# Performance work log

Measured on AMD Instinct MI355X. Metric: run time of the kernel, lower is better.

## Reference

```python
import jax, jax.numpy as jnp
import numpy as np


def _pointnet(x, w1, b1, w2, b2, w3, b3):
    # x: [B, P, 5] -> pointwise MLP then max-pool over points -> [B, 64]
    h = jax.nn.relu(x @ w1.T + b1)
    h = jax.nn.relu(h @ w2.T + b2)
    h = h @ w3.T + b3
    return h.max(axis=1)


def _lstm_layer(x, wih, whh, bih, bhh):
    # x: [B, T, D]; PyTorch gate order i, f, g, o
    B = x.shape[0]
    H = whh.shape[1]
    def step(carry, xt):
        h, c = carry
        g = xt @ wih.T + bih + h @ whh.T + bhh
        i, f, gg, o = jnp.split(g, 4, axis=-1)
        c = jax.nn.sigmoid(f) * c + jax.nn.sigmoid(i) * jnp.tanh(gg)
        h = jax.nn.sigmoid(o) * jnp.tanh(c)
        return (h, c), h
    init = (jnp.zeros((B, H), x.dtype), jnp.zeros((B, H), x.dtype))
    (h_last, _), hs = jax.lax.scan(step, init, jnp.swapaxes(x, 0, 1))
    return jnp.swapaxes(hs, 0, 1), h_last


def _edge_conv(h, mask, wt, bt, wp, bp):
    # DGL EdgeConv: h_i' = max_{j in N(i)} theta(h_j - h_i) + phi(h_i)
    # theta is linear -> max_j (Th_j) - Th_i + b_theta + phi(h_i)
    Th = h @ wt.T                       # [V,128]
    Ph = h @ wp.T + bp                  # [V,128]
    neigh_max = jnp.max(jnp.where(mask[:, :, None], Th[None, :, :], -jnp.inf), axis=1)
    return neigh_max - Th + bt + Ph


def _edge_regr(e, w1, b1, w2, b2):
    return jax.nn.sigmoid(jax.nn.relu(e @ w1.T + b1) @ w2.T + b2)


def _affinity(h, N, M, er_w1, er_b1, er_w2, er_b2):
    # faithful to source: edges[i*M+j] = h[j] - h[i]  (j indexes first M rows, as in the code)
    E = (h[None, :M, :] - h[:N, None, :]).reshape(N * M, -1)
    return _edge_regr(E, er_w1, er_b1, er_w2, er_b2).reshape(N, M)


def setup_inputs() -> dict:
    key = jax.random.key(0)
    ks = iter(jax.random.split(key, 40))
    N, M, P, T = 256, 256, 512, 10
    lin = lambda k, o, i: (jax.random.normal(k, (o, i), jnp.float32) / np.sqrt(i)).astype(jnp.float32)
    inp = {
        'det_pts': jax.random.normal(next(ks), (N, P, 5), jnp.float32),
        'det_boxes': jax.random.normal(next(ks), (N, 9), jnp.float32),
        'track_pts': jax.random.normal(next(ks), (M, P, 5), jnp.float32),
        'track_boxes': jax.random.normal(next(ks), (M, T, 9), jnp.float32),
        'adj': jax.random.randint(next(ks), (N + M, N + M), 0, 2, jnp.int32),
        'pn_w1': lin(next(ks), 64, 5), 'pn_b1': jnp.zeros((64,), jnp.float32),
        'pn_w2': lin(next(ks), 128, 64), 'pn_b2': jnp.zeros((128,), jnp.float32),
        'pn_w3': lin(next(ks), 64, 128), 'pn_b3': jnp.zeros((64,), jnp.float32),
        'dm_w1': lin(next(ks), 32, 9), 'dm_b1': jnp.zeros((32,), jnp.float32),
        'dm_w2': lin(next(ks), 64, 32), 'dm_b2': jnp.zeros((64,), jnp.float32),
        'l0_wih': lin(next(ks), 256, 9), 'l0_whh': lin(next(ks), 256, 64),
        'l0_bih': jnp.zeros((256,), jnp.float32), 'l0_bhh': jnp.zeros((256,), jnp.float32),
        'l1_wih': lin(next(ks), 256, 64), 'l1_whh': lin(next(ks), 256, 64),
        'l1_bih': jnp.zeros((256,), jnp.float32), 'l1_bhh': jnp.zeros((256,), jnp.float32),
        'gc_wt': jnp.stack([lin(next(ks), 128, 128) for _ in range(4)]),
        'gc_bt': jnp.zeros((4, 128), jnp.float32),
        'gc_wp': jnp.stack([lin(next(ks), 128, 128) for _ in range(4)]),
        'gc_bp': jnp.zeros((4, 128), jnp.float32),
        'er_w1': lin(next(ks), 64, 128), 'er_b1': jnp.zeros((64,), jnp.float32),
        'er_w2': lin(next(ks), 1, 64), 'er_b2': jnp.zeros((1,), jnp.float32),
    }
    return inp


def reference(det_pts, det_boxes, track_pts, track_boxes, adj,
              pn_w1, pn_b1, pn_w2, pn_b2, pn_w3, pn_b3,
              dm_w1, dm_b1, dm_w2, dm_b2,
              l0_wih, l0_whh, l0_bih, l0_bhh,
              l1_wih, l1_whh, l1_bih, l1_bhh,
              gc_wt, gc_bt, gc_wp, gc_bp,
              er_w1, er_b1, er_w2, er_b2):
    N, M = det_pts.shape[0], track_pts.shape[0]
    V = N + M
    # appearance features (shared PointNet)
    det_app = _pointnet(det_pts, pn_w1, pn_b1, pn_w2, pn_b2, pn_w3, pn_b3)    # [N,64]
    trk_app = _pointnet(track_pts, pn_w1, pn_b1, pn_w2, pn_b2, pn_w3, pn_b3)  # [M,64]
    # motion features
    det_mot = jax.nn.relu(det_boxes @ dm_w1.T + dm_b1) @ dm_w2.T + dm_b2      # [N,64]
    hs0, _ = _lstm_layer(track_boxes, l0_wih, l0_whh, l0_bih, l0_bhh)
    _, trk_mot = _lstm_layer(hs0, l1_wih, l1_whh, l1_bih, l1_bhh)             # [M,64]
    h = jnp.concatenate([
        jnp.concatenate([det_app, det_mot], axis=1),
        jnp.concatenate([trk_app, trk_mot], axis=1)], axis=0)                 # [V,128]
    # neighbor-source mask: edge i->j for adj[i,j]!=0, plus self-loops
    mask = (adj.T != 0) | jnp.eye(V, dtype=bool)                              # mask[i,j]: j is source neighbor of i
    aff1 = None
    for k in range(4):
        h = jax.nn.relu(_edge_conv(h, mask, gc_wt[k], gc_bt[k], gc_wp[k], gc_bp[k]))
        if k == 0:
            aff1 = _affinity(h, N, M, er_w1, er_b1, er_w2, er_b2)
    aff_final = _affinity(h, N, M, er_w1, er_b1, er_w2, er_b2)
    return jnp.stack([aff1, aff_final])  # [2, N, M]
```

## Files before the change

### kernel.cpp

```cpp
#include <hip/hip_runtime.h>
#include <math.h>

#define NDET 256
#define NTRK 256
#define NV   512
#define PPTS 512

typedef short bf16x8 __attribute__((ext_vector_type(8)));
typedef float f32x4  __attribute__((ext_vector_type(4)));

__device__ __forceinline__ float sigf(float x) { return 1.f / (1.f + __expf(-x)); }
__device__ __forceinline__ float ftanh(float x) {
    const float xc = fmaxf(fminf(x, 15.f), -15.f);
    const float e = __expf(2.f * xc);
    return (e - 1.f) / (e + 1.f);
}

__device__ __forceinline__ short f2bf(float f) {
    unsigned u = __float_as_uint(f);
    u += 0x7fffu + ((u >> 16) & 1u);
    return (short)(u >> 16);
}
__device__ __forceinline__ unsigned pack2bf(float lo, float hi) {
    return (unsigned)(unsigned short)f2bf(lo) | ((unsigned)(unsigned short)f2bf(hi) << 16);
}
__device__ __forceinline__ bf16x8 load_frag_bf16(const float* __restrict__ src) {
    const float4 a = *(const float4*)src;
    const float4 b = *(const float4*)(src + 4);
    bf16x8 r;
    r[0] = f2bf(a.x); r[1] = f2bf(a.y); r[2] = f2bf(a.z); r[3] = f2bf(a.w);
    r[4] = f2bf(b.x); r[5] = f2bf(b.y); r[6] = f2bf(b.z); r[7] = f2bf(b.w);
    return r;
}

__global__ __launch_bounds__(256) void pointnet_kernel(
    const float* __restrict__ det_pts, const float* __restrict__ track_pts,
    const float* __restrict__ w1, const float* __restrict__ b1,
    const float* __restrict__ w2, const float* __restrict__ b2,
    const float* __restrict__ w3, const float* __restrict__ b3,
    const float* __restrict__ det_boxes,
    const float* __restrict__ dw1, const float* __restrict__ db1,
    const float* __restrict__ dw2, const float* __restrict__ db2,
    float* __restrict__ hout)
{
    __shared__ __align__(16) short sH1[64][72];
    __shared__ __align__(16) short sH2[64][136];
    __shared__ __align__(16) float sX[320];
    __shared__ float sW1f[64][6];
    __shared__ float sB1[64];
    __shared__ float sbox[9];
    __shared__ float sh32[32];

    const int t  = threadIdx.x;
    const int b  = blockIdx.x;
    const int w  = t >> 6;
    const int ln = t & 15;
    const int kq = (t >> 4) & 3;
    const float* x = (b < NDET) ? (det_pts + (size_t)b * PPTS * 5)
                                : (track_pts + (size_t)(b - NDET) * PPTS * 5);

    for (int i = t; i < 320; i += 256) sW1f[i / 5][i % 5] = w1[i];
    if (t < 64) sB1[t] = b1[t];

    bf16x8 bf2[2][2];
#pragma unroll
    for (int nt = 0; nt < 2; ++nt)
#pragma unroll
        for (int Kt = 0; Kt < 2; ++Kt)
            bf2[nt][Kt] = load_frag_bf16(w2 + (size_t)(32 * w + 16 * nt + ln) * 64 + kq * 8 + 32 * Kt);
    bf16x8 bf3[4];
#pragma unroll
    for (int Kt = 0; Kt < 4; ++Kt)
        bf3[Kt] = load_frag_bf16(w3 + (size_t)(16 * w + ln) * 128 + kq * 8 + 32 * Kt);
    float bn[2];
#pragma unroll
    for (int nt = 0; nt < 2; ++nt) bn[nt] = b2[32 * w + 16 * nt + ln];
    __syncthreads();

    float runmax[4] = {-1e30f, -1e30f, -1e30f, -1e30f};

    const int pt = t & 63;
    for (int c = 0; c < PPTS / 64; ++c) {
        for (int i = t; i < 320; i += 256) sX[i] = x[c * 320 + i];
        __syncthreads();
        {
            float xv[5];
#pragma unroll
            for (int k = 0; k < 5; ++k) xv[k] = sX[pt * 5 + k];
#pragma unroll
            for (int jj = 0; jj < 8; ++jj) {
                const int d0 = w * 16 + 2 * jj;
                float a0 = sB1[d0], a1 = sB1[d0 + 1];
#pragma unroll
                for (int k = 0; k < 5; ++k) {
                    a0 = fmaf(xv[k], sW1f[d0][k], a0);
                    a1 = fmaf(xv[k], sW1f[d0 + 1][k], a1);
                }
                *(unsigned*)&sH1[pt][d0] = pack2bf(fmaxf(a0, 0.f), fmaxf(a1, 0.f));
            }
        }
        __syncthreads();
        {
            bf16x8 af[4][2];
#pragma unroll
            for (int Mt = 0; Mt < 4; ++Mt)
#pragma unroll
                for (int Kt = 0; Kt < 2; ++Kt)
                    af[Mt][Kt] = *(const bf16x8*)&sH1[16 * Mt + ln][kq * 8 + 32 * Kt];
#pragma unroll
            for (int Mt = 0; Mt < 4; ++Mt) {
#pragma unroll
                for (int nt = 0; nt < 2; ++nt) {
                    f32x4 cacc = {0.f, 0.f, 0.f, 0.f};
                    cacc = __builtin_amdgcn_mfma_f32_16x16x32_bf16(af[Mt][0], bf2[nt][0], cacc, 0, 0, 0);
                    cacc = __builtin_amdgcn_mfma_f32_16x16x32_bf16(af[Mt][1], bf2[nt][1], cacc, 0, 0, 0);
                    const int col = 32 * w + 16 * nt + ln;
#pragma unroll
                    for (int r = 0; r < 4; ++r)
                        sH2[16 * Mt + kq * 4 + r][col] = f2bf(fmaxf(cacc[r] + bn[nt], 0.f));
                }
            }
        }
        __syncthreads();
        {
#pragma unroll
            for (int Mt = 0; Mt < 4; ++Mt) {
                f32x4 cacc = {0.f, 0.f, 0.f, 0.f};
#pragma unroll
                for (int Kt = 0; Kt < 4; ++Kt) {
                    const bf16x8 a = *(const bf16x8*)&sH2[16 * Mt + ln][kq * 8 + 32 * Kt];
                    cacc = __builtin_amdgcn_mfma_f32_16x16x32_bf16(a, bf3[Kt], cacc, 0, 0, 0);
                }
#pragma unroll
                for (int r = 0; r < 4; ++r) runmax[r] = fmaxf(runmax[r], cacc[r]);
            }
        }
        __syncthreads();
    }

    float rm = fmaxf(fmaxf(runmax[0], runmax[1]), fmaxf(runmax[2], runmax[3]));
    rm = fmaxf(rm, __shfl_xor(rm, 16));
    rm = fmaxf(rm, __shfl_xor(rm, 32));
    if ((t & 63) < 16) {
        const int n = 16 * w + ln;
        hout[b * 128 + n] = rm + b3[n];
    }

    if (b < NDET) {
        if (t < 9) sbox[t] = det_boxes[b * 9 + t];
        __syncthreads();
        if (t < 32) {
            float a = db1[t];
#pragma unroll
            for (int k = 0; k < 9; ++k) a = fmaf(dw1[t * 9 + k], sbox[k], a);
            sh32[t] = fmaxf(a, 0.f);
        }
        __syncthreads();
        if (t < 64) {
            float a = db2[t];
#pragma unroll
            for (int k = 0; k < 32; ++k) a = fmaf(dw2[t * 32 + k], sh32[k], a);
            hout[b * 128 + 64 + t] = a;
        }
    }
}

__global__ __launch_bounds__(256, 1) void lstm_kernel(
    const float* __restrict__ track_boxes,
    const float* __restrict__ wih0, const float* __restrict__ whh0,
    const float* __restrict__ bih0, const float* __restrict__ bhh0,
    const float* __restrict__ wih1, const float* __restrict__ whh1,
    const float* __restrict__ bih1, const float* __restrict__ bhh1,
    float* __restrict__ hout)
{
    __shared__ float sx[90];
    __shared__ float sg[256];
    __shared__ __align__(16) float sh0[64];
    __shared__ __align__(16) float sh1[64];

    const int t = threadIdx.x;
    const int m = blockIdx.x;
    const int u = t & 63;

    if (t < 90) sx[t] = track_boxes[m * 90 + t];
    if (t < 64) { sh0[t] = 0.f; sh1[t] = 0.f; }

    float w0[9];
#pragma unroll
    for (int k = 0; k < 9; ++k) w0[k] = wih0[t * 9 + k];
    float4 wr0[16], wi1[16], wr1[16];
    {
        const float4* p0 = (const float4*)(whh0 + t * 64);
        const float4* p1 = (const float4*)(wih1 + t * 64);
        const float4* p2 = (const float4*)(whh1 + t * 64);
#pragma unroll
        for (int k = 0; k < 16; ++k) { wr0[k] = p0[k]; wi1[k] = p1[k]; wr1[k] = p2[k]; }
    }
    const float bias0 = bih0[t] + bhh0[t];
    const float bias1 = bih1[t] + bhh1[t];

    float c0 = 0.f, c1 = 0.f, h1reg = 0.f;
    __syncthreads();

    for (int s = 0; s < 10; ++s) {
        {
            float acc0 = bias0, acc1 = 0.f, acc2 = 0.f, acc3 = 0.f;
#pragma unroll
            for (int k = 0; k < 9; ++k) acc0 = fmaf(w0[k], sx[s * 9 + k], acc0);
            const float4* hv = (const float4*)sh0;
#pragma unroll
            for (int k = 0; k < 16; k += 4) {
                float4 hA = hv[k], hB = hv[k + 1], hC = hv[k + 2], hD = hv[k + 3];
                acc0 = fmaf(wr0[k].x, hA.x, acc0); acc0 = fmaf(wr0[k].y, hA.y, acc0);
                acc0 = fmaf(wr0[k].z, hA.z, acc0); acc0 = fmaf(wr0[k].w, hA.w, acc0);
                acc1 = fmaf(wr0[k+1].x, hB.x, acc1); acc1 = fmaf(wr0[k+1].y, hB.y, acc1);
                acc1 = fmaf(wr0[k+1].z, hB.z, acc1); acc1 = fmaf(wr0[k+1].w, hB.w, acc1);
                acc2 = fmaf(wr0[k+2].x, hC.x, acc2); acc2 = fmaf(wr0[k+2].y, hC.y, acc2);
                acc2 = fmaf(wr0[k+2].z, hC.z, acc2); acc2 = fmaf(wr0[k+2].w, hC.w, acc2);
                acc3 = fmaf(wr0[k+3].x, hD.x, acc3); acc3 = fmaf(wr0[k+3].y, hD.y, acc3);
                acc3 = fmaf(wr0[k+3].z, hD.z, acc3); acc3 = fmaf(wr0[k+3].w, hD.w, acc3);
            }
            sg[t] = (acc0 + acc1) + (acc2 + acc3);
        }
        __syncthreads();
        if (t < 64) {
            const float gi = sg[u], gf = sg[64 + u], gg = sg[128 + u], go = sg[192 + u];
            c0 = sigf(gf) * c0 + sigf(gi) * ftanh(gg);
            sh0[u] = sigf(go) * ftanh(c0);
        }
        __syncthreads();
        {
            float acc0 = bias1, acc1 = 0.f, acc2 = 0.f, acc3 = 0.f;
            const float4* xv = (const float4*)sh0;
            const float4* hv = (const float4*)sh1;
#pragma unroll
            for (int k = 0; k < 16; k += 4) {
                float4 xA = xv[k], xB = xv[k + 1], xC = xv[k + 2], xD = xv[k + 3];
                acc0 = fmaf(wi1[k].x, xA.x, acc0); acc0 = fmaf(wi1[k].y, xA.y, acc0);
                acc0 = fmaf(wi1[k].z, xA.z, acc0); acc0 = fmaf(wi1[k].w, xA.w, acc0);
                acc1 = fmaf(wi1[k+1].x, xB.x, acc1); acc1 = fmaf(wi1[k+1].y, xB.y, acc1);
                acc1 = fmaf(wi1[k+1].z, xB.z, acc1); acc1 = fmaf(wi1[k+1].w, xB.w, acc1);
                acc2 = fmaf(wi1[k+2].x, xC.x, acc2); acc2 = fmaf(wi1[k+2].y, xC.y, acc2);
                acc2 = fmaf(wi1[k+2].z, xC.z, acc2); acc2 = fmaf(wi1[k+2].w, xC.w, acc2);
                acc3 = fmaf(wi1[k+3].x, xD.x, acc3); acc3 = fmaf(wi1[k+3].y, xD.y, acc3);
                acc3 = fmaf(wi1[k+3].z, xD.z, acc3); acc3 = fmaf(wi1[k+3].w, xD.w, acc3);
            }
#pragma unroll
            for (int k = 0; k < 16; k += 4) {
                float4 hA = hv[k], hB = hv[k + 1], hC = hv[k + 2], hD = hv[k + 3];
                acc0 = fmaf(wr1[k].x, hA.x, acc0); acc0 = fmaf(wr1[k].y, hA.y, acc0);
                acc0 = fmaf(wr1[k].z, hA.z, acc0); acc0 = fmaf(wr1[k].w, hA.w, acc0);
                acc1 = fmaf(wr1[k+1].x, hB.x, acc1); acc1 = fmaf(wr1[k+1].y, hB.y, acc1);
                acc1 = fmaf(wr1[k+1].z, hB.z, acc1); acc1 = fmaf(wr1[k+1].w, hB.w, acc1);
                acc2 = fmaf(wr1[k+2].x, hC.x, acc2); acc2 = fmaf(wr1[k+2].y, hC.y, acc2);
                acc2 = fmaf(wr1[k+2].z, hC.z, acc2); acc2 = fmaf(wr1[k+2].w, hC.w, acc2);
                acc3 = fmaf(wr1[k+3].x, hD.x, acc3); acc3 = fmaf(wr1[k+3].y, hD.y, acc3);
                acc3 = fmaf(wr1[k+3].z, hD.z, acc3); acc3 = fmaf(wr1[k+3].w, hD.w, acc3);
            }
            sg[t] = (acc0 + acc1) + (acc2 + acc3);
        }
        __syncthreads();
        if (t < 64) {
            const float gi = sg[u], gf = sg[64 + u], gg = sg[128 + u], go = sg[192 + u];
            c1 = sigf(gf) * c1 + sigf(gi) * ftanh(gg);
            h1reg = sigf(go) * ftanh(c1);
            sh1[u] = h1reg;
        }
        __syncthreads();
    }

    if (t < 64) hout[(size_t)(NDET + m) * 128 + 64 + u] = h1reg;
}

__global__ __launch_bounds__(128) void econv_gemm_kernel(
    const float* __restrict__ hin, const float* __restrict__ wt,
    const float* __restrict__ wp, const float* __restrict__ bp,
    float* __restrict__ Th, float* __restrict__ Ph)
{
    __shared__ __align__(16) float srow[128];
    const int t = threadIdx.x, v = blockIdx.x;
    srow[t] = hin[v * 128 + t];
    __syncthreads();
    const float4* hr = (const float4*)srow;
    const float4* wtr = (const float4*)(wt + t * 128);
    const float4* wpr = (const float4*)(wp + t * 128);
    float aT = 0.f, aP = bp[t];
#pragma unroll 8
    for (int k = 0; k < 32; ++k) {
        const float4 h = hr[k];
        const float4 a = wtr[k];
        aT = fmaf(a.x, h.x, aT); aT = fmaf(a.y, h.y, aT);
        aT = fmaf(a.z, h.z, aT); aT = fmaf(a.w, h.w, aT);
        const float4 b = wpr[k];
        aP = fmaf(b.x, h.x, aP); aP = fmaf(b.y, h.y, aP);
        aP = fmaf(b.z, h.z, aP); aP = fmaf(b.w, h.w, aP);
    }
    Th[v * 128 + t] = aT;
    Ph[v * 128 + t] = aP;
}

__global__ __launch_bounds__(128) void econv_fused_kernel(
    const int* __restrict__ adj, const float* __restrict__ Th,
    const float* __restrict__ Ph, const float* __restrict__ bt,
    const float* __restrict__ wtn, const float* __restrict__ wpn,
    const float* __restrict__ bpn,
    const float* __restrict__ erw1, float* __restrict__ uu,
    float* __restrict__ Thn, float* __restrict__ Phn)
{
    __shared__ float sneg[NV];
    __shared__ __align__(16) float4 sred[4][32];
    __shared__ __align__(16) float sh[128];

    const int t = threadIdx.x, i = blockIdx.x;
    const int l32 = t & 31, grp = t >> 5;

    for (int j = t; j < NV; j += 128)
        sneg[j] = ((adj[j * NV + i] != 0) || (j == i)) ? 0.f : -3e38f;

    const float thi = Th[i * 128 + t];
    const float phi = Ph[i * 128 + t];
    const float btv = bt[t];
    __syncthreads();

    float4 mx = {-3e38f, -3e38f, -3e38f, -3e38f};
    const float* __restrict__ thp = Th + 4 * l32;
#pragma unroll 4
    for (int jb = 0; jb < NV; jb += 16) {
        float4 v[4];
#pragma unroll
        for (int jj = 0; jj < 4; ++jj)
            v[jj] = *(const float4*)&thp[(size_t)(jb + 4 * jj + grp) * 128];
#pragma unroll
        for (int jj = 0; jj < 4; ++jj) {
            const float s = sneg[jb + 4 * jj + grp];
            mx.x = fmaxf(mx.x, v[jj].x + s);
            mx.y = fmaxf(mx.y, v[jj].y + s);
            mx.z = fmaxf(mx.z, v[jj].z + s);
            mx.w = fmaxf(mx.w, v[jj].w + s);
        }
    }
    sred[grp][l32] = mx;
    __syncthreads();

    const float* rf = (const float*)sred;
    const float m = fmaxf(fmaxf(rf[t], rf[128 + t]), fmaxf(rf[256 + t], rf[384 + t]));
    sh[t] = fmaxf(m - thi + btv + phi, 0.f);
    __syncthreads();

    const float4* hr = (const float4*)sh;
    if (wtn) {
        const float4* wtr = (const float4*)(wtn + t * 128);
        const float4* wpr = (const float4*)(wpn + t * 128);
        float aT = 0.f, aP = bpn[t];
#pragma unroll 8
        for (int k = 0; k < 32; ++k) {
            const float4 h = hr[k];
            const float4 a = wtr[k];
            aT = fmaf(a.x, h.x, aT); aT = fmaf(a.y, h.y, aT);
            aT = fmaf(a.z, h.z, aT); aT = fmaf(a.w, h.w, aT);
            const float4 b = wpr[k];
            aP = fmaf(b.x, h.x, aP); aP = fmaf(b.y, h.y, aP);
            aP = fmaf(b.z, h.z, aP); aP = fmaf(b.w, h.w, aP);
        }
        Thn[i * 128 + t] = aT;
        Phn[i * 128 + t] = aP;
    }
    if (erw1 && i < NDET && t < 64) {
        const float4* wr = (const float4*)(erw1 + t * 128);
        float a = 0.f;
#pragma unroll 8
        for (int k = 0; k < 32; ++k) {
            const float4 h = hr[k], wv = wr[k];
            a = fmaf(wv.x, h.x, a); a = fmaf(wv.y, h.y, a);
            a = fmaf(wv.z, h.z, a); a = fmaf(wv.w, h.w, a);
        }
        uu[i * 64 + t] = a;
    }
}

__global__ __launch_bounds__(256) void edge_kernel(
    const float* __restrict__ uu1, const float* __restrict__ uu2,
    const float* __restrict__ b1, const float* __restrict__ w2,
    const float* __restrict__ b2, float* __restrict__ out)
{
    __shared__ float sui[64], sw2[64], sb1[64];
    const int t = threadIdx.x, blk = blockIdx.x;
    const float* u = (blk < NDET) ? uu1 : uu2;
    float* o = (blk < NDET) ? out : out + NDET * NTRK;
    const int i = blk & (NDET - 1);
    if (t < 64) { sui[t] = u[i * 64 + t]; sw2[t] = w2[t]; sb1[t] = b1[t]; }
    __syncthreads();
    const float4* ur = (const float4*)(u + t * 64);
    float a = b2[0];
#pragma unroll
    for (int k = 0; k < 16; ++k) {
        const float4 uv = ur[k];
        const int k4 = k * 4;
        a = fmaf(sw2[k4 + 0], fmaxf(uv.x - sui[k4 + 0] + sb1[k4 + 0], 0.f), a);
        a = fmaf(sw2[k4 + 1], fmaxf(uv.y - sui[k4 + 1] + sb1[k4 + 1], 0.f), a);
        a = fmaf(sw2[k4 + 2], fmaxf(uv.z - sui[k4 + 2] + sb1[k4 + 2], 0.f), a);
        a = fmaf(sw2[k4 + 3], fmaxf(uv.w - sui[k4 + 3] + sb1[k4 + 3], 0.f), a);
    }
    o[i * 256 + t] = 1.f / (1.f + __expf(-a));
}

extern "C" void kernel_launch(void* const* d_in, const int* in_sizes, int n_in,
                              void* d_out, int out_size, void* d_ws, size_t ws_size,
                              hipStream_t stream)
{
    const float* det_pts     = (const float*)d_in[0];
    const float* det_boxes   = (const float*)d_in[1];
    const float* track_pts   = (const float*)d_in[2];
    const float* track_boxes = (const float*)d_in[3];
    const int*   adj         = (const int*)d_in[4];
    const float* pn_w1 = (const float*)d_in[5],  *pn_b1 = (const float*)d_in[6];
    const float* pn_w2 = (const float*)d_in[7],  *pn_b2 = (const float*)d_in[8];
    const float* pn_w3 = (const float*)d_in[9],  *pn_b3 = (const float*)d_in[10];
    const float* dm_w1 = (const float*)d_in[11], *dm_b1 = (const float*)d_in[12];
    const float* dm_w2 = (const float*)d_in[13], *dm_b2 = (const float*)d_in[14];
    const float* l0_wih = (const float*)d_in[15], *l0_whh = (const float*)d_in[16];
    const float* l0_bih = (const float*)d_in[17], *l0_bhh = (const float*)d_in[18];
    const float* l1_wih = (const float*)d_in[19], *l1_whh = (const float*)d_in[20];
    const float* l1_bih = (const float*)d_in[21], *l1_bhh = (const float*)d_in[22];
    const float* gc_wt = (const float*)d_in[23], *gc_bt = (const float*)d_in[24];
    const float* gc_wp = (const float*)d_in[25], *gc_bp = (const float*)d_in[26];
    const float* er_w1 = (const float*)d_in[27], *er_b1 = (const float*)d_in[28];
    const float* er_w2 = (const float*)d_in[29], *er_b2 = (const float*)d_in[30];
    float* out = (float*)d_out;

    float* hA  = (float*)d_ws;
    float* Th  = hA  + NV * 128;
    float* Ph  = Th  + NV * 128;
    float* Th2 = Ph  + NV * 128;
    float* Ph2 = Th2 + NV * 128;
    float* uu1 = Ph2 + NV * 128;
    float* uu2 = uu1 + NDET * 64;

    pointnet_kernel<<<NV, 256, 0, stream>>>(det_pts, track_pts,
        pn_w1, pn_b1, pn_w2, pn_b2, pn_w3, pn_b3,
        det_boxes, dm_w1, dm_b1, dm_w2, dm_b2, hA);
    lstm_kernel<<<NTRK, 256, 0, stream>>>(track_boxes,
        l0_wih, l0_whh, l0_bih, l0_bhh, l1_wih, l1_whh, l1_bih, l1_bhh, hA);

    econv_gemm_kernel<<<NV, 128, 0, stream>>>(hA, gc_wt, gc_wp, gc_bp, Th, Ph);

    const size_t WSZ = 128 * 128;
    econv_fused_kernel<<<NV, 128, 0, stream>>>(adj, Th, Ph, gc_bt,
        gc_wt + WSZ, gc_wp + WSZ, gc_bp + 128, er_w1, uu1, Th2, Ph2);
    econv_fused_kernel<<<NV, 128, 0, stream>>>(adj, Th2, Ph2, gc_bt + 128,
        gc_wt + 2 * WSZ, gc_wp + 2 * WSZ, gc_bp + 256, nullptr, nullptr, Th, Ph);
    econv_fused_kernel<<<NV, 128, 0, stream>>>(adj, Th, Ph, gc_bt + 256,
        gc_wt + 3 * WSZ, gc_wp + 3 * WSZ, gc_bp + 384, nullptr, nullptr, Th2, Ph2);
    econv_fused_kernel<<<NV, 128, 0, stream>>>(adj, Th2, Ph2, gc_bt + 384,
        nullptr, nullptr, nullptr, er_w1, uu2, nullptr, nullptr);

    edge_kernel<<<NV, 256, 0, stream>>>(uu1, uu2, er_b1, er_w2, er_b2, out);
}
```

Baseline: 244.1 us.

## Merge edge-conv and affinity stages into one cooperative kernel with grid syncs

Replaces the six launches for the graph-conv layers and the affinity edge kernel with a single cooperative kernel of 512 blocks. Grid-wide syncs separate the layers, and each block keeps its adjacency mask in shared memory across all four layers, so it is read once instead of four times. Each block's own Th/Ph row stays in registers. The aim is to remove launch overhead and repeated mask loads. In exchange it adds five grid barriers and a cooperative launch, and the final edge stage now runs with 128 threads doing two outputs each.

```diff
diff --git a/kernel.cpp b/kernel.cpp
--- a/kernel.cpp
+++ b/kernel.cpp
@@ -1,5 +1,8 @@
 #include <hip/hip_runtime.h>
+#include <hip/hip_cooperative_groups.h>
 #include <math.h>
+
+namespace cg = cooperative_groups;
 
 #define NDET 256
 #define NTRK 256
@@ -272,86 +275,40 @@
     if (t < 64) hout[(size_t)(NDET + m) * 128 + 64 + u] = h1reg;
 }
 
-__global__ __launch_bounds__(128) void econv_gemm_kernel(
-    const float* __restrict__ hin, const float* __restrict__ wt,
-    const float* __restrict__ wp, const float* __restrict__ bp,
-    float* __restrict__ Th, float* __restrict__ Ph)
+__global__ void backend_kernel(
+    const float* __restrict__ hA, const int* __restrict__ adj,
+    const float* __restrict__ gc_wt, const float* __restrict__ gc_bt,
+    const float* __restrict__ gc_wp, const float* __restrict__ gc_bp,
+    const float* __restrict__ er_w1, const float* __restrict__ er_b1,
+    const float* __restrict__ er_w2, const float* __restrict__ er_b2,
+    float* __restrict__ ThA, float* __restrict__ PhA,
+    float* __restrict__ ThB, float* __restrict__ PhB,
+    float* __restrict__ uu1, float* __restrict__ uu2,
+    float* __restrict__ out)
 {
+    cg::grid_group grid = cg::this_grid();
+
     __shared__ __align__(16) float srow[128];
-    const int t = threadIdx.x, v = blockIdx.x;
-    srow[t] = hin[v * 128 + t];
-    __syncthreads();
-    const float4* hr = (const float4*)srow;
-    const float4* wtr = (const float4*)(wt + t * 128);
-    const float4* wpr = (const float4*)(wp + t * 128);
-    float aT = 0.f, aP = bp[t];
-#pragma unroll 8
-    for (int k = 0; k < 32; ++k) {
-        const float4 h = hr[k];
-        const float4 a = wtr[k];
-        aT = fmaf(a.x, h.x, aT); aT = fmaf(a.y, h.y, aT);
-        aT = fmaf(a.z, h.z, aT); aT = fmaf(a.w, h.w, aT);
-        const float4 b = wpr[k];
-        aP = fmaf(b.x, h.x, aP); aP = fmaf(b.y, h.y, aP);
-        aP = fmaf(b.z, h.z, aP); aP = fmaf(b.w, h.w, aP);
-    }
-    Th[v * 128 + t] = aT;
-    Ph[v * 128 + t] = aP;
-}
-
-__global__ __launch_bounds__(128) void econv_fused_kernel(
-    const int* __restrict__ adj, const float* __restrict__ Th,
-    const float* __restrict__ Ph, const float* __restrict__ bt,
-    const float* __restrict__ wtn, const float* __restrict__ wpn,
-    const float* __restrict__ bpn,
-    const float* __restrict__ erw1, float* __restrict__ uu,
-    float* __restrict__ Thn, float* __restrict__ Phn)
-{
     __shared__ float sneg[NV];
     __shared__ __align__(16) float4 sred[4][32];
     __shared__ __align__(16) float sh[128];
+    __shared__ float sui[64], sw2v[64], sb1v[64];
 
     const int t = threadIdx.x, i = blockIdx.x;
     const int l32 = t & 31, grp = t >> 5;
+    const size_t WSZ = 128 * 128;
 
     for (int j = t; j < NV; j += 128)
         sneg[j] = ((adj[j * NV + i] != 0) || (j == i)) ? 0.f : -3e38f;
 
-    const float thi = Th[i * 128 + t];
-    const float phi = Ph[i * 128 + t];
-    const float btv = bt[t];
+    srow[t] = hA[(size_t)i * 128 + t];
     __syncthreads();
-
-    float4 mx = {-3e38f, -3e38f, -3e38f, -3e38f};
-    const float* __restrict__ thp = Th + 4 * l32;
-#pragma unroll 4
-    for (int jb = 0; jb < NV; jb += 16) {
-        float4 v[4];
-#pragma unroll
-        for (int jj = 0; jj < 4; ++jj)
-            v[jj] = *(const float4*)&thp[(size_t)(jb + 4 * jj + grp) * 128];
-#pragma unroll
-        for (int jj = 0; jj < 4; ++jj) {
-            const float s = sneg[jb + 4 * jj + grp];
-            mx.x = fmaxf(mx.x, v[jj].x + s);
-            mx.y = fmaxf(mx.y, v[jj].y + s);
-            mx.z = fmaxf(mx.z, v[jj].z + s);
-            mx.w = fmaxf(mx.w, v[jj].w + s);
-        }
-    }
-    sred[grp][l32] = mx;
-    __syncthreads();
-
-    const float* rf = (const float*)sred;
-    const float m = fmaxf(fmaxf(rf[t], rf[128 + t]), fmaxf(rf[256 + t], rf[384 + t]));
-    sh[t] = fmaxf(m - thi + btv + phi, 0.f);
-    __syncthreads();
-
-    const float4* hr = (const float4*)sh;
-    if (wtn) {
-        const float4* wtr = (const float4*)(wtn + t * 128);
-        const float4* wpr = (const float4*)(wpn + t * 128);
-        float aT = 0.f, aP = bpn[t];
+    float thi, phi;
+    {
+        const float4* hr = (const float4*)srow;
+        const float4* wtr = (const float4*)(gc_wt + (size_t)t * 128);
+        const float4* wpr = (const float4*)(gc_wp + (size_t)t * 128);
+        float aT = 0.f, aP = gc_bp[t];
 #pragma unroll 8
         for (int k = 0; k < 32; ++k) {
             const float4 h = hr[k];
@@ -362,46 +319,103 @@
             aP = fmaf(b.x, h.x, aP); aP = fmaf(b.y, h.y, aP);
             aP = fmaf(b.z, h.z, aP); aP = fmaf(b.w, h.w, aP);
         }
-        Thn[i * 128 + t] = aT;
-        Phn[i * 128 + t] = aP;
-    }
-    if (erw1 && i < NDET && t < 64) {
-        const float4* wr = (const float4*)(erw1 + t * 128);
-        float a = 0.f;
+        ThA[(size_t)i * 128 + t] = aT;
+        PhA[(size_t)i * 128 + t] = aP;
+        thi = aT; phi = aP;
+    }
+    grid.sync();
+
+    float* Tin = ThA; float* Tout = ThB;
+    float* Pout = PhB;
+    for (int k = 0; k < 4; ++k) {
+        const bool active = (k < 3) || (i < NDET);
+        if (active) {
+            const float btv = gc_bt[k * 128 + t];
+            float4 mx = {-3e38f, -3e38f, -3e38f, -3e38f};
+            const float* __restrict__ thp = Tin + 4 * l32;
+#pragma unroll 4
+            for (int jb = 0; jb < NV; jb += 16) {
+                float4 v[4];
+#pragma unroll
+                for (int jj = 0; jj < 4; ++jj)
+                    v[jj] = *(const float4*)&thp[(size_t)(jb + 4 * jj + grp) * 128];
+#pragma unroll
+                for (int jj = 0; jj < 4; ++jj) {
+                    const float s = sneg[jb + 4 * jj + grp];
+                    mx.x = fmaxf(mx.x, v[jj].x + s);
+                    mx.y = fmaxf(mx.y, v[jj].y + s);
+                    mx.z = fmaxf(mx.z, v[jj].z + s);
+                    mx.w = fmaxf(mx.w, v[jj].w + s);
+                }
+            }
+            sred[grp][l32] = mx;
+            __syncthreads();
+
+            const float* rf = (const float*)sred;
+            const float m = fmaxf(fmaxf(rf[t], rf[128 + t]), fmaxf(rf[256 + t], rf[384 + t]));
+            sh[t] = fmaxf(m - thi + btv + phi, 0.f);
+            __syncthreads();
+
+            const float4* hr = (const float4*)sh;
+            if (k < 3) {
+                const float* wtn = gc_wt + (size_t)(k + 1) * WSZ;
+                const float* wpn = gc_wp + (size_t)(k + 1) * WSZ;
+                const float4* wtr = (const float4*)(wtn + (size_t)t * 128);
+                const float4* wpr = (const float4*)(wpn + (size_t)t * 128);
+                float aT = 0.f, aP = gc_bp[(k + 1) * 128 + t];
 #pragma unroll 8
-        for (int k = 0; k < 32; ++k) {
-            const float4 h = hr[k], wv = wr[k];
-            a = fmaf(wv.x, h.x, a); a = fmaf(wv.y, h.y, a);
-            a = fmaf(wv.z, h.z, a); a = fmaf(wv.w, h.w, a);
-        }
-        uu[i * 64 + t] = a;
-    }
-}
-
-__global__ __launch_bounds__(256) void edge_kernel(
-    const float* __restrict__ uu1, const float* __restrict__ uu2,
-    const float* __restrict__ b1, const float* __restrict__ w2,
-    const float* __restrict__ b2, float* __restrict__ out)
-{
-    __shared__ float sui[64], sw2[64], sb1[64];
-    const int t = threadIdx.x, blk = blockIdx.x;
-    const float* u = (blk < NDET) ? uu1 : uu2;
-    float* o = (blk < NDET) ? out : out + NDET * NTRK;
-    const int i = blk & (NDET - 1);
-    if (t < 64) { sui[t] = u[i * 64 + t]; sw2[t] = w2[t]; sb1[t] = b1[t]; }
+                for (int kk = 0; kk < 32; ++kk) {
+                    const float4 h = hr[kk];
+                    const float4 a = wtr[kk];
+                    aT = fmaf(a.x, h.x, aT); aT = fmaf(a.y, h.y, aT);
+                    aT = fmaf(a.z, h.z, aT); aT = fmaf(a.w, h.w, aT);
+                    const float4 b = wpr[kk];
+                    aP = fmaf(b.x, h.x, aP); aP = fmaf(b.y, h.y, aP);
+                    aP = fmaf(b.z, h.z, aP); aP = fmaf(b.w, h.w, aP);
+                }
+                Tout[(size_t)i * 128 + t] = aT;
+                Pout[(size_t)i * 128 + t] = aP;
+                thi = aT; phi = aP;
+            }
+            if ((k == 0 || k == 3) && i < NDET && t < 64) {
+                float* uu = (k == 0) ? uu1 : uu2;
+                const float4* wr = (const float4*)(er_w1 + (size_t)t * 128);
+                float a = 0.f;
+#pragma unroll 8
+                for (int kk = 0; kk < 32; ++kk) {
+                    const float4 h = hr[kk], wv = wr[kk];
+                    a = fmaf(wv.x, h.x, a); a = fmaf(wv.y, h.y, a);
+                    a = fmaf(wv.z, h.z, a); a = fmaf(wv.w, h.w, a);
+                }
+                uu[(size_t)i * 64 + t] = a;
+            }
+        }
+        float* tmp = Tin; Tin = Tout; Tout = tmp;
+        Pout = (Pout == PhB) ? PhA : PhB;
+        grid.sync();
+    }
+
+    const int row = i & (NDET - 1);
+    const float* u = (i < NDET) ? uu1 : uu2;
+    float* o = (i < NDET) ? out : out + NDET * NTRK;
+    if (t < 64) { sui[t] = u[row * 64 + t]; sw2v[t] = er_w2[t]; sb1v[t] = er_b1[t]; }
     __syncthreads();
-    const float4* ur = (const float4*)(u + t * 64);
-    float a = b2[0];
-#pragma unroll
-    for (int k = 0; k < 16; ++k) {
-        const float4 uv = ur[k];
-        const int k4 = k * 4;
-        a = fmaf(sw2[k4 + 0], fmaxf(uv.x - sui[k4 + 0] + sb1[k4 + 0], 0.f), a);
-        a = fmaf(sw2[k4 + 1], fmaxf(uv.y - sui[k4 + 1] + sb1[k4 + 1], 0.f), a);
-        a = fmaf(sw2[k4 + 2], fmaxf(uv.z - sui[k4 + 2] + sb1[k4 + 2], 0.f), a);
-        a = fmaf(sw2[k4 + 3], fmaxf(uv.w - sui[k4 + 3] + sb1[k4 + 3], 0.f), a);
-    }
-    o[i * 256 + t] = 1.f / (1.f + __expf(-a));
+#pragma unroll
+    for (int jj = 0; jj < 2; ++jj) {
+        const int j = t + 128 * jj;
+        const float4* ur = (const float4*)(u + (size_t)j * 64);
+        float a = er_b2[0];
+#pragma unroll
+        for (int k = 0; k < 16; ++k) {
+            const float4 uv = ur[k];
+            const int k4 = k * 4;
+            a = fmaf(sw2v[k4 + 0], fmaxf(uv.x - sui[k4 + 0] + sb1v[k4 + 0], 0.f), a);
+            a = fmaf(sw2v[k4 + 1], fmaxf(uv.y - sui[k4 + 1] + sb1v[k4 + 1], 0.f), a);
+            a = fmaf(sw2v[k4 + 2], fmaxf(uv.z - sui[k4 + 2] + sb1v[k4 + 2], 0.f), a);
+            a = fmaf(sw2v[k4 + 3], fmaxf(uv.w - sui[k4 + 3] + sb1v[k4 + 3], 0.f), a);
+        }
+        o[row * 256 + j] = 1.f / (1.f + __expf(-a));
+    }
 }
 
 extern "C" void kernel_launch(void* const* d_in, const int* in_sizes, int n_in,
@@ -442,17 +456,13 @@
     lstm_kernel<<<NTRK, 256, 0, stream>>>(track_boxes,
         l0_wih, l0_whh, l0_bih, l0_bhh, l1_wih, l1_whh, l1_bih, l1_bhh, hA);
 
-    econv_gemm_kernel<<<NV, 128, 0, stream>>>(hA, gc_wt, gc_wp, gc_bp, Th, Ph);
-
-    const size_t WSZ = 128 * 128;
-    econv_fused_kernel<<<NV, 128, 0, stream>>>(adj, Th, Ph, gc_bt,
-        gc_wt + WSZ, gc_wp + WSZ, gc_bp + 128, er_w1, uu1, Th2, Ph2);
-    econv_fused_kernel<<<NV, 128, 0, stream>>>(adj, Th2, Ph2, gc_bt + 128,
-        gc_wt + 2 * WSZ, gc_wp + 2 * WSZ, gc_bp + 256, nullptr, nullptr, Th, Ph);
-    econv_fused_kernel<<<NV, 128, 0, stream>>>(adj, Th, Ph, gc_bt + 256,
-        gc_wt + 3 * WSZ, gc_wp + 3 * WSZ, gc_bp + 384, nullptr, nullptr, Th2, Ph2);
-    econv_fused_kernel<<<NV, 128, 0, stream>>>(adj, Th2, Ph2, gc_bt + 384,
-        nullptr, nullptr, nullptr, er_w1, uu2, nullptr, nullptr);
-
-    edge_kernel<<<NV, 256, 0, stream>>>(uu1, uu2, er_b1, er_w2, er_b2, out);
-}
+    void* args[] = {
+        (void*)&hA, (void*)&adj,
+        (void*)&gc_wt, (void*)&gc_bt, (void*)&gc_wp, (void*)&gc_bp,
+        (void*)&er_w1, (void*)&er_b1, (void*)&er_w2, (void*)&er_b2,
+        (void*)&Th, (void*)&Ph, (void*)&Th2, (void*)&Ph2,
+        (void*)&uu1, (void*)&uu2, (void*)&out
+    };
+    hipLaunchCooperativeKernel((const void*)backend_kernel,
+                               dim3(NV), dim3(128), args, 0, stream);
+}
```

Result: slower. 518.5 us (+112.4%).

## Split PointNet across two blocks per object and widen edge-conv blocks to 256 threads

Applied to the files above, without the earlier changes.

PointNet now launches two blocks per object, each handling half of the points and writing a partial max without the bias. The combine step (max of the two halves plus b3) moves into econv_gemm_kernel's row load. The edge-conv fused kernel goes to 256 threads: the neighbor max is spread over 8 groups, and the Th and Ph projections are split across the two thread halves. The aim is more parallelism in both phases, which were latency-bound at 512 blocks. The cost is an extra partial-result buffer and a wider 8-way reduction.

```diff
diff --git a/kernel.cpp b/kernel.cpp
--- a/kernel.cpp
+++ b/kernel.cpp
@@ -37,11 +37,11 @@
     const float* __restrict__ det_pts, const float* __restrict__ track_pts,
     const float* __restrict__ w1, const float* __restrict__ b1,
     const float* __restrict__ w2, const float* __restrict__ b2,
-    const float* __restrict__ w3, const float* __restrict__ b3,
+    const float* __restrict__ w3,
     const float* __restrict__ det_boxes,
     const float* __restrict__ dw1, const float* __restrict__ db1,
     const float* __restrict__ dw2, const float* __restrict__ db2,
-    float* __restrict__ hout)
+    float* __restrict__ pp, float* __restrict__ hout)
 {
     __shared__ __align__(16) short sH1[64][72];
     __shared__ __align__(16) short sH2[64][136];
@@ -52,12 +52,14 @@
     __shared__ float sh32[32];
 
     const int t  = threadIdx.x;
-    const int b  = blockIdx.x;
+    const int bb = blockIdx.x >> 1;
+    const int s  = blockIdx.x & 1;
     const int w  = t >> 6;
     const int ln = t & 15;
     const int kq = (t >> 4) & 3;
-    const float* x = (b < NDET) ? (det_pts + (size_t)b * PPTS * 5)
-                                : (track_pts + (size_t)(b - NDET) * PPTS * 5);
+    const float* x = ((bb < NDET) ? (det_pts + (size_t)bb * PPTS * 5)
+                                  : (track_pts + (size_t)(bb - NDET) * PPTS * 5))
+                     + (size_t)s * 1280;
 
     for (int i = t; i < 320; i += 256) sW1f[i / 5][i % 5] = w1[i];
     if (t < 64) sB1[t] = b1[t];
@@ -80,7 +82,7 @@
     float runmax[4] = {-1e30f, -1e30f, -1e30f, -1e30f};
 
     const int pt = t & 63;
-    for (int c = 0; c < PPTS / 64; ++c) {
+    for (int c = 0; c < 4; ++c) {
         for (int i = t; i < 320; i += 256) sX[i] = x[c * 320 + i];
         __syncthreads();
         {
@@ -143,11 +145,11 @@
     rm = fmaxf(rm, __shfl_xor(rm, 32));
     if ((t & 63) < 16) {
         const int n = 16 * w + ln;
-        hout[b * 128 + n] = rm + b3[n];
-    }
-
-    if (b < NDET) {
-        if (t < 9) sbox[t] = det_boxes[b * 9 + t];
+        pp[(size_t)blockIdx.x * 64 + n] = rm;
+    }
+
+    if (bb < NDET && s == 0) {
+        if (t < 9) sbox[t] = det_boxes[bb * 9 + t];
         __syncthreads();
         if (t < 32) {
             float a = db1[t];
@@ -160,7 +162,7 @@
             float a = db2[t];
 #pragma unroll
             for (int k = 0; k < 32; ++k) a = fmaf(dw2[t * 32 + k], sh32[k], a);
-            hout[b * 128 + 64 + t] = a;
+            hout[(size_t)bb * 128 + 64 + t] = a;
         }
     }
 }
@@ -273,13 +275,16 @@
 }
 
 __global__ __launch_bounds__(128) void econv_gemm_kernel(
+    const float* __restrict__ pp, const float* __restrict__ b3,
     const float* __restrict__ hin, const float* __restrict__ wt,
     const float* __restrict__ wp, const float* __restrict__ bp,
     float* __restrict__ Th, float* __restrict__ Ph)
 {
     __shared__ __align__(16) float srow[128];
     const int t = threadIdx.x, v = blockIdx.x;
-    srow[t] = hin[v * 128 + t];
+    srow[t] = (t < 64)
+        ? fmaxf(pp[(size_t)v * 128 + t], pp[(size_t)v * 128 + 64 + t]) + b3[t]
+        : hin[(size_t)v * 128 + t];
     __syncthreads();
     const float4* hr = (const float4*)srow;
     const float4* wtr = (const float4*)(wt + t * 128);
@@ -299,7 +304,7 @@
     Ph[v * 128 + t] = aP;
 }
 
-__global__ __launch_bounds__(128) void econv_fused_kernel(
+__global__ __launch_bounds__(256) void econv_fused_kernel(
     const int* __restrict__ adj, const float* __restrict__ Th,
     const float* __restrict__ Ph, const float* __restrict__ bt,
     const float* __restrict__ wtn, const float* __restrict__ wpn,
@@ -308,31 +313,34 @@
     float* __restrict__ Thn, float* __restrict__ Phn)
 {
     __shared__ float sneg[NV];
-    __shared__ __align__(16) float4 sred[4][32];
+    __shared__ __align__(16) float4 sred[8][32];
     __shared__ __align__(16) float sh[128];
 
     const int t = threadIdx.x, i = blockIdx.x;
     const int l32 = t & 31, grp = t >> 5;
 
-    for (int j = t; j < NV; j += 128)
+    for (int j = t; j < NV; j += 256)
         sneg[j] = ((adj[j * NV + i] != 0) || (j == i)) ? 0.f : -3e38f;
 
-    const float thi = Th[i * 128 + t];
-    const float phi = Ph[i * 128 + t];
-    const float btv = bt[t];
+    float thi = 0.f, phi = 0.f, btv = 0.f;
+    if (t < 128) {
+        thi = Th[i * 128 + t];
+        phi = Ph[i * 128 + t];
+        btv = bt[t];
+    }
     __syncthreads();
 
     float4 mx = {-3e38f, -3e38f, -3e38f, -3e38f};
     const float* __restrict__ thp = Th + 4 * l32;
 #pragma unroll 4
-    for (int jb = 0; jb < NV; jb += 16) {
+    for (int jb = 0; jb < NV; jb += 32) {
         float4 v[4];
 #pragma unroll
         for (int jj = 0; jj < 4; ++jj)
-            v[jj] = *(const float4*)&thp[(size_t)(jb + 4 * jj + grp) * 128];
+            v[jj] = *(const float4*)&thp[(size_t)(jb + 4 * grp + jj) * 128];
 #pragma unroll
         for (int jj = 0; jj < 4; ++jj) {
-            const float s = sneg[jb + 4 * jj + grp];
+            const float s = sneg[jb + 4 * grp + jj];
             mx.x = fmaxf(mx.x, v[jj].x + s);
             mx.y = fmaxf(mx.y, v[jj].y + s);
             mx.z = fmaxf(mx.z, v[jj].z + s);
@@ -342,31 +350,32 @@
     sred[grp][l32] = mx;
     __syncthreads();
 
-    const float* rf = (const float*)sred;
-    const float m = fmaxf(fmaxf(rf[t], rf[128 + t]), fmaxf(rf[256 + t], rf[384 + t]));
-    sh[t] = fmaxf(m - thi + btv + phi, 0.f);
+    if (t < 128) {
+        const float* rf = (const float*)sred;
+        float m = rf[t];
+#pragma unroll
+        for (int g = 1; g < 8; ++g) m = fmaxf(m, rf[g * 128 + t]);
+        sh[t] = fmaxf(m - thi + btv + phi, 0.f);
+    }
     __syncthreads();
 
     const float4* hr = (const float4*)sh;
     if (wtn) {
-        const float4* wtr = (const float4*)(wtn + t * 128);
-        const float4* wpr = (const float4*)(wpn + t * 128);
-        float aT = 0.f, aP = bpn[t];
+        const int d = t & 127;
+        const float* wsrc = (t < 128) ? wtn : wpn;
+        const float4* wr = (const float4*)(wsrc + (size_t)d * 128);
+        float acc = (t < 128) ? 0.f : bpn[d];
 #pragma unroll 8
         for (int k = 0; k < 32; ++k) {
-            const float4 h = hr[k];
-            const float4 a = wtr[k];
-            aT = fmaf(a.x, h.x, aT); aT = fmaf(a.y, h.y, aT);
-            aT = fmaf(a.z, h.z, aT); aT = fmaf(a.w, h.w, aT);
-            const float4 b = wpr[k];
-            aP = fmaf(b.x, h.x, aP); aP = fmaf(b.y, h.y, aP);
-            aP = fmaf(b.z, h.z, aP); aP = fmaf(b.w, h.w, aP);
-        }
-        Thn[i * 128 + t] = aT;
-        Phn[i * 128 + t] = aP;
+            const float4 h = hr[k], wv = wr[k];
+            acc = fmaf(wv.x, h.x, acc); acc = fmaf(wv.y, h.y, acc);
+            acc = fmaf(wv.z, h.z, acc); acc = fmaf(wv.w, h.w, acc);
+        }
+        if (t < 128) Thn[i * 128 + d] = acc;
+        else         Phn[i * 128 + d] = acc;
     }
     if (erw1 && i < NDET && t < 64) {
-        const float4* wr = (const float4*)(erw1 + t * 128);
+        const float4* wr = (const float4*)(erw1 + (size_t)t * 128);
         float a = 0.f;
 #pragma unroll 8
         for (int k = 0; k < 32; ++k) {
@@ -435,23 +444,25 @@
     float* Ph2 = Th2 + NV * 128;
     float* uu1 = Ph2 + NV * 128;
     float* uu2 = uu1 + NDET * 64;
-
-    pointnet_kernel<<<NV, 256, 0, stream>>>(det_pts, track_pts,
-        pn_w1, pn_b1, pn_w2, pn_b2, pn_w3, pn_b3,
-        det_boxes, dm_w1, dm_b1, dm_w2, dm_b2, hA);
+    float* pp  = uu2 + NDET * 64;
+
+    pointnet_kernel<<<2 * NV, 256, 0, stream>>>(det_pts, track_pts,
+        pn_w1, pn_b1, pn_w2, pn_b2, pn_w3,
+        det_boxes, dm_w1, dm_b1, dm_w2, dm_b2, pp, hA);
     lstm_kernel<<<NTRK, 256, 0, stream>>>(track_boxes,
         l0_wih, l0_whh, l0_bih, l0_bhh, l1_wih, l1_whh, l1_bih, l1_bhh, hA);
 
-    econv_gemm_kernel<<<NV, 128, 0, stream>>>(hA, gc_wt, gc_wp, gc_bp, Th, Ph);
+    econv_gemm_kernel<<<NV, 128, 0, stream>>>(pp, pn_b3, hA,
+        gc_wt, gc_wp, gc_bp, Th, Ph);
 
     const size_t WSZ = 128 * 128;
-    econv_fused_kernel<<<NV, 128, 0, stream>>>(adj, Th, Ph, gc_bt,
+    econv_fused_kernel<<<NV, 256, 0, stream>>>(adj, Th, Ph, gc_bt,
         gc_wt + WSZ, gc_wp + WSZ, gc_bp + 128, er_w1, uu1, Th2, Ph2);
-    econv_fused_kernel<<<NV, 128, 0, stream>>>(adj, Th2, Ph2, gc_bt + 128,
+    econv_fused_kernel<<<NV, 256, 0, stream>>>(adj, Th2, Ph2, gc_bt + 128,
         gc_wt + 2 * WSZ, gc_wp + 2 * WSZ, gc_bp + 256, nullptr, nullptr, Th, Ph);
-    econv_fused_kernel<<<NV, 128, 0, stream>>>(adj, Th, Ph, gc_bt + 256,
+    econv_fused_kernel<<<NV, 256, 0, stream>>>(adj, Th, Ph, gc_bt + 256,
         gc_wt + 3 * WSZ, gc_wp + 3 * WSZ, gc_bp + 384, nullptr, nullptr, Th2, Ph2);
-    econv_fused_kernel<<<NV, 128, 0, stream>>>(adj, Th2, Ph2, gc_bt + 384,
+    econv_fused_kernel<<<NV, 256, 0, stream>>>(adj, Th2, Ph2, gc_bt + 384,
         nullptr, nullptr, nullptr, er_w1, uu2, nullptr, nullptr);
 
     edge_kernel<<<NV, 256, 0, stream>>>(uu1, uu2, er_b1, er_w2, er_b2, out);
```

Measured after the change: 237.8 us. 1.03x faster.
